# Performance work log

Hardware: AMD Instinct MI355X
Metric: run time of the kernel (lower is better)

The kernel has to match this reference:

```python
import jax, jax.numpy as jnp
import numpy as np

D, H, DK, DF = 512, 8, 64, 2048  # dim, heads, head_dim, forward_dim
EPS = 1e-5


def _layernorm(x, g, b):
    mu = jnp.mean(x, axis=-1, keepdims=True)
    var = jnp.mean(jnp.square(x - mu), axis=-1, keepdims=True)
    return (x - mu) * jax.lax.rsqrt(var + EPS) * g + b


def setup_inputs() -> dict:
    key = jax.random.key(0)
    ks = jax.random.split(key, 16)
    B, S = 2, 2048
    s_in = 1.0 / np.sqrt(D)
    s_ff = 1.0 / np.sqrt(DF)
    s_cat = 1.0 / np.sqrt(H * DK)
    return {
        "x": jax.random.normal(ks[0], (B, S, D), jnp.float32),
        # per-head Q/K/V projections stacked over heads: [H, D, DK]
        "Wq": jax.random.uniform(ks[1], (H, D, DK), jnp.float32, -s_in, s_in),
        "bq": jax.random.uniform(ks[2], (H, DK), jnp.float32, -s_in, s_in),
        "Wk": jax.random.uniform(ks[3], (H, D, DK), jnp.float32, -s_in, s_in),
        "bk": jax.random.uniform(ks[4], (H, DK), jnp.float32, -s_in, s_in),
        "Wv": jax.random.uniform(ks[5], (H, D, DK), jnp.float32, -s_in, s_in),
        "bv": jax.random.uniform(ks[6], (H, DK), jnp.float32, -s_in, s_in),
        "Wo": jax.random.uniform(ks[7], (H * DK, D), jnp.float32, -s_cat, s_cat),
        "bo": jax.random.uniform(ks[8], (D,), jnp.float32, -s_cat, s_cat),
        "ln1_g": jnp.ones((D,), jnp.float32),
        "ln1_b": jnp.zeros((D,), jnp.float32),
        "W1": jax.random.uniform(ks[9], (D, DF), jnp.float32, -s_in, s_in),
        "b1": jax.random.uniform(ks[10], (DF,), jnp.float32, -s_in, s_in),
        "W2": jax.random.uniform(ks[11], (DF, D), jnp.float32, -s_ff, s_ff),
        "b2": jax.random.uniform(ks[12], (D,), jnp.float32, -s_ff, s_ff),
        "ln2_g": jnp.ones((D,), jnp.float32),
        "ln2_b": jnp.zeros((D,), jnp.float32),
    }


def reference(x, Wq, bq, Wk, bk, Wv, bv, Wo, bo, ln1_g, ln1_b, W1, b1, W2, b2, ln2_g, ln2_b):
    # Per-head projections, batched over heads: [B,H,S,DK]
    q = jnp.einsum('bsd,hdk->bhsk', x, Wq) + bq[None, :, None, :]
    k = jnp.einsum('bsd,hdk->bhsk', x, Wk) + bk[None, :, None, :]
    v = jnp.einsum('bsd,hdk->bhsk', x, Wv) + bv[None, :, None, :]
    scale = 1.0 / np.sqrt(DK)
    scores = jnp.einsum('bhsk,bhtk->bhst', q, k) * scale  # [B,H,S,S]
    attn = jax.nn.softmax(scores, axis=-1)
    o = jnp.einsum('bhst,bhtk->bhsk', attn, v)  # [B,H,S,DK]
    # concat heads (head order matches torch cat over ModuleList)
    B, _, S, _ = o.shape
    o = o.transpose(0, 2, 1, 3).reshape(B, S, H * DK)
    attn_out = o @ Wo + bo
    # Residual 1 (dropout = identity in eval): LN(x + sublayer(x))
    h = _layernorm(x + attn_out, ln1_g, ln1_b)
    # FeedForward + Residual 2
    ff = jax.nn.relu(h @ W1 + b1) @ W2 + b2
    return _layernorm(h + ff, ln2_g, ln2_b)
```

## Files before the change

kernel.cpp:

```cpp
#include <hip/hip_runtime.h>


#define Dm   512
#define Hh   8
#define DKk  64
#define DFf  2048
#define Bb   2
#define Ss   2048
#define Nn   4096

typedef __attribute__((ext_vector_type(8))) short short8;
typedef __attribute__((ext_vector_type(4))) float f32x4;
typedef __attribute__((ext_vector_type(4))) short short4v;
typedef __attribute__((ext_vector_type(2))) int   int2v;

__device__ inline float bf2f(short s) {
    unsigned u = ((unsigned)(unsigned short)s) << 16;
    float f; __builtin_memcpy(&f, &u, 4); return f;
}
__device__ inline short f2bf(float f) {
    unsigned u; __builtin_memcpy(&u, &f, 4);
    u = (u + 0x7fff + ((u >> 16) & 1)) >> 16;
    return (short)u;
}
__device__ inline short cvt_elem(const void* p, long i, int f32flag) {
    if (f32flag) return f2bf(((const float*)p)[i]);
    return ((const short*)p)[i];
}
__device__ inline int detect_f32(const void* x) {
    const float* xf = (const float*)x;
    int ok = 0;
#pragma unroll
    for (int i = 0; i < 16; ++i) {
        float a = fabsf(xf[i]);
        ok += (a > 1e-8f && a < 1e4f) ? 1 : 0;
    }
    return ok >= 8;
}
__device__ inline void gload_lds16(const short* g, short* l) {
    __builtin_amdgcn_global_load_lds(
        (const __attribute__((address_space(1))) unsigned int*)g,
        (__attribute__((address_space(3))) unsigned int*)l, 16, 0, 0);
}

__device__ inline void epi_store128(
    short* SM, const f32x4 (&acc)[4][4], const short* bias, int colbias,
    short* out, long rowbase, long pitch, int colbase,
    float scale, int relu, int wm, int wn, int quad, int l15, int t)
{
    __syncthreads();
#pragma unroll
    for (int nt = 0; nt < 4; ++nt) {
        int col_l = wn * 64 + nt * 16 + l15;
        float bb = bias ? bf2f(bias[colbias + col_l]) : 0.f;
#pragma unroll
        for (int mt = 0; mt < 4; ++mt)
#pragma unroll
            for (int r = 0; r < 4; ++r) {
                int row_l = wm * 64 + mt * 16 + quad * 4 + r;
                float v = (acc[mt][nt][r] + bb) * scale;
                if (relu) v = fmaxf(v, 0.f);
                SM[row_l * 136 + col_l] = f2bf(v);
            }
    }
    __syncthreads();
    int row_l = t >> 1;
    int x0 = (t & 1) * 64;
#pragma unroll
    for (int k = 0; k < 8; ++k)
        *(short8*)&out[(rowbase + row_l) * pitch + colbase + x0 + k * 8] =
            *(const short8*)&SM[row_l * 136 + x0 + k * 8];
}

__global__ __launch_bounds__(256) void prep_kernel(
    const void* __restrict__ x, short* __restrict__ xb,
    const void* bq, const void* bk, const void* bv, const void* bo,
    const void* b1, const void* b2, const void* g1, const void* be1,
    const void* g2, const void* be2, short* __restrict__ smalls,
    const void* Wq, const void* Wk, const void* Wv,
    const void* Wo, const void* W1, const void* W2,
    short* __restrict__ WqkvT,
    short* __restrict__ WoT, short* __restrict__ W1T, short* __restrict__ W2T)
{
    const int f = detect_f32(x);
    int blk = blockIdx.x;
    if (blk < 512) {
        long base = (long)blk * 4096;
        if (!f) {
            const short8* src8 = (const short8*)((const short*)x + base);
            short8* dst8 = (short8*)(xb + base);
            for (int i = threadIdx.x; i < 512; i += 256) dst8[i] = src8[i];
        } else {
            for (int i = threadIdx.x; i < 4096; i += 256)
                xb[base + i] = cvt_elem(x, base + i, f);
        }
        return;
    }
    if (blk == 512) {
        const void* srcs[10] = {bq, bk, bv, bo, b1, b2, g1, be1, g2, be2};
        const int   sz[10]   = {512, 512, 512, 512, 2048, 512, 512, 512, 512, 512};
        int off = 0;
        for (int j = 0; j < 10; ++j) {
            for (int i = threadIdx.x; i < sz[j]; i += 256)
                smalls[off + i] = cvt_elem(srcs[j], i, f);
            off += sz[j];
        }
        return;
    }
    __shared__ short tile[64][65];
    blk -= 513;
    const void* src; short* dst; long srcoff = 0; long dstoff = 0; int R, C, tr, tc;
    if (blk < 192) {
        int m = blk >> 6; int r = blk & 63; int h = r >> 3; int t = r & 7;
        src = (m == 0) ? Wq : (m == 1) ? Wk : Wv;
        dst = WqkvT + (long)m * 512 * 512;
        srcoff = (long)h * 512 * 64; dstoff = (long)h * 64 * 512;
        R = 512; C = 64; tr = t; tc = 0;
    } else if (blk < 256) {
        int r = blk - 192; src = Wo; dst = WoT; R = 512; C = 512; tr = r >> 3; tc = r & 7;
    } else if (blk < 512) {
        int r = blk - 256; src = W1; dst = W1T; R = 512; C = 2048; tr = r >> 5; tc = r & 31;
    } else {
        int r = blk - 512; src = W2; dst = W2T; R = 2048; C = 512; tr = r >> 3; tc = r & 7;
    }
    int r0 = tr * 64, c0 = tc * 64;
    if (!f) {
        const short* s16 = (const short*)src;
        for (int i = threadIdx.x; i < 512; i += 256) {
            int rr = i >> 3, c8 = (i & 7) * 8;
            short8 v = *(const short8*)&s16[srcoff + (long)(r0 + rr) * C + c0 + c8];
#pragma unroll
            for (int j = 0; j < 8; ++j) tile[rr][c8 + j] = v[j];
        }
        __syncthreads();
        for (int i = threadIdx.x; i < 512; i += 256) {
            int cc = i >> 3, r8 = (i & 7) * 8;
            short8 w;
#pragma unroll
            for (int j = 0; j < 8; ++j) w[j] = tile[r8 + j][cc];
            *(short8*)&dst[dstoff + (long)(c0 + cc) * R + r0 + r8] = w;
        }
    } else {
        for (int i = threadIdx.x; i < 4096; i += 256) {
            int rr = i >> 6, cc = i & 63;
            tile[rr][cc] = cvt_elem(src, srcoff + (long)(r0 + rr) * C + c0 + cc, f);
        }
        __syncthreads();
        for (int i = threadIdx.x; i < 4096; i += 256) {
            int cc = i >> 6, rr = i & 63;
            dst[dstoff + (long)(c0 + cc) * R + r0 + rr] = tile[rr][cc];
        }
    }
}

#define MODE_PART      1
#define MODE_RELU_BF16 2
#define MODE_QKV       4

__global__ __launch_bounds__(256) void gemm_kernel(
    const short* __restrict__ A, const short* __restrict__ Bt,
    const short* __restrict__ bias, void* __restrict__ outp,
    void* __restrict__ out2, void* __restrict__ out3,
    int K, int Ncols, int mode, int Ktile)
{
    __shared__ __align__(16) short SMEM[32768];
    short* As = SMEM;
    short* Bs = SMEM + 16384;
    const int t    = threadIdx.x;
    const int lane = t & 63;
    const int wave = t >> 6;
    const int quad = lane >> 4;
    const int l15  = lane & 15;
    const int wm = wave >> 1, wn = wave & 1;
    const int row0 = blockIdx.x * 128;
    const int col0 = blockIdx.y * 128;
    const int kbase = blockIdx.z * Ktile;

    const int ri = lane >> 3;
    const int ct = (lane & 7) ^ ri;

    f32x4 acc[4][4];
#pragma unroll
    for (int i = 0; i < 4; ++i)
#pragma unroll
        for (int j = 0; j < 4; ++j) acc[i][j] = (f32x4){0.f, 0.f, 0.f, 0.f};

    auto stage = [&](int buf, int k0) {
#pragma unroll
        for (int p = 0; p < 4; ++p) {
            int r = wave * 32 + p * 8;
            gload_lds16(A + (long)(row0 + r + ri) * K + kbase + k0 + ct * 8,
                        &As[buf * 8192 + r * 64 + lane * 8]);
        }
#pragma unroll
        for (int p = 0; p < 4; ++p) {
            int r = wave * 32 + p * 8;
            gload_lds16(Bt + (long)(col0 + r + ri) * K + kbase + k0 + ct * 8,
                        &Bs[buf * 8192 + r * 64 + lane * 8]);
        }
    };

    stage(0, 0);
    int cur = 0;
    const int niter = Ktile >> 6;
    for (int it = 0; it < niter; ++it) {
        asm volatile("s_waitcnt vmcnt(0)" ::: "memory");
        __syncthreads();
        if (it + 1 < niter) stage(cur ^ 1, (it + 1) * 64);
#pragma unroll
        for (int kk = 0; kk < 2; ++kk) {
            short8 af[4], bfr[4];
#pragma unroll
            for (int mt = 0; mt < 4; ++mt) {
                int rowa = wm * 64 + mt * 16 + l15;
                af[mt] = *(const short8*)&As[cur * 8192 + rowa * 64
                              + (((kk * 4 + quad) ^ (rowa & 7)) * 8)];
            }
#pragma unroll
            for (int nt = 0; nt < 4; ++nt) {
                int rowb = wn * 64 + nt * 16 + l15;
                bfr[nt] = *(const short8*)&Bs[cur * 8192 + rowb * 64
                              + (((kk * 4 + quad) ^ (rowb & 7)) * 8)];
            }
#pragma unroll
            for (int mt = 0; mt < 4; ++mt)
#pragma unroll
                for (int nt = 0; nt < 4; ++nt)
                    acc[mt][nt] = __builtin_amdgcn_mfma_f32_16x16x32_bf16(
                        af[mt], bfr[nt], acc[mt][nt], 0, 0, 0);
        }
        cur ^= 1;
    }

    if (mode == MODE_QKV) {
        if (col0 < 1024) {
            int m = col0 >> 9;
            short* out = (short*)(m == 0 ? outp : out2);
            float sc = (m == 0) ? 0.125f : 1.0f;
            epi_store128(SMEM, acc, bias, col0, out, row0, 512, col0 & 511,
                         sc, 0, wm, wn, quad, l15, t);
        } else {
            __syncthreads();
            short* Asf = SMEM;
#pragma unroll
            for (int nt = 0; nt < 4; ++nt) {
                int col_l = wn * 64 + nt * 16 + l15;
                float bb = bf2f(bias[col0 + col_l]);
#pragma unroll
                for (int mt = 0; mt < 4; ++mt) {
                    int row4 = wm * 16 + mt * 4 + quad;
                    int slot = row4 ^ (col_l & 31);
                    short4v pk;
#pragma unroll
                    for (int r = 0; r < 4; ++r) pk[r] = f2bf(acc[mt][nt][r] + bb);
                    *(short4v*)&Asf[col_l * 128 + slot * 4] = pk;
                }
            }
            __syncthreads();
            short* out = (short*)out3;
            int col_l = t >> 1;
            int cl = col0 + col_l - 1024;
            int hh = cl >> 6, kk2 = cl & 63;
            int bg = row0 >> 11;
            long obase = ((long)(bg * Hh + hh) * DKk + kk2) * Ss + (row0 & 2047);
#pragma unroll
            for (int i = 0; i < 8; ++i) {
                int chunk = (t & 1) * 8 + i;
                int s0 = (chunk * 2)     ^ (col_l & 31);
                int s1 = (chunk * 2 + 1) ^ (col_l & 31);
                short4v a = *(const short4v*)&Asf[col_l * 128 + s0 * 4];
                short4v b4 = *(const short4v*)&Asf[col_l * 128 + s1 * 4];
                short8 w;
                w[0] = a[0];  w[1] = a[1];  w[2] = a[2];  w[3] = a[3];
                w[4] = b4[0]; w[5] = b4[1]; w[6] = b4[2]; w[7] = b4[3];
                *(short8*)&out[obase + chunk * 8] = w;
            }
        }
    } else if (mode == MODE_PART) {
        short* out = (short*)outp + (long)blockIdx.z * Nn * Ncols;
        epi_store128(SMEM, acc, (blockIdx.z == 0) ? bias : nullptr, col0,
                     out, row0, Ncols, col0, 1.f, 0, wm, wn, quad, l15, t);
    } else {
        epi_store128(SMEM, acc, bias, col0, (short*)outp, row0, Ncols, col0,
                     1.f, 1, wm, wn, quad, l15, t);
    }
}

__global__ __launch_bounds__(256) void wogemm_kernel(
    const short* __restrict__ po, const float* __restrict__ ls,
    const short* __restrict__ Bt, const short* __restrict__ bias,
    short* __restrict__ outp)
{
    __shared__ __align__(16) short SMEM[32768];
    short* As = SMEM;
    short* Bs = SMEM + 16384;
    const int t    = threadIdx.x;
    const int lane = t & 63;
    const int wave = t >> 6;
    const int quad = lane >> 4;
    const int l15  = lane & 15;
    const int wm = wave >> 1, wn = wave & 1;
    const int row0 = blockIdx.x * 128;
    const int col0 = blockIdx.y * 128;
    const int z    = blockIdx.z;

    const int ri = lane >> 3;
    const int ct = (lane & 7) ^ ri;
    const int myrow = t >> 1;
    const int tcb = (t & 1) * 4;
    const int bg = row0 >> 11;
    const int qtl = (row0 >> 7) & 15;

    f32x4 acc[4][4];
#pragma unroll
    for (int i = 0; i < 4; ++i)
#pragma unroll
        for (int j = 0; j < 4; ++j) acc[i][j] = (f32x4){0.f, 0.f, 0.f, 0.f};

    auto stageB = [&](int buf, int k0) {
#pragma unroll
        for (int p = 0; p < 4; ++p) {
            int r = wave * 32 + p * 8;
            gload_lds16(Bt + (long)(col0 + r + ri) * 512 + z * 256 + k0 + ct * 8,
                        &Bs[buf * 8192 + r * 64 + lane * 8]);
        }
    };

    short8 aR[4][4];
    float  lR[4];
    auto loadA = [&](int it) {
        int h = z * 4 + it;
        long pbase = ((long)(bg * Hh + h) * 16 + qtl) * 4;
#pragma unroll
        for (int ks = 0; ks < 4; ++ks) {
            lR[ks] = ls[(pbase + ks) * 128 + myrow];
#pragma unroll
            for (int c = 0; c < 4; ++c)
                aR[c][ks] = *(const short8*)&po[((pbase + ks) * 128 + myrow) * 64
                                                + (tcb + c) * 8];
        }
    };
    auto cvtwrite = [&](int buf) {
        float invL = __builtin_amdgcn_rcpf(lR[0] + lR[1] + lR[2] + lR[3]);
#pragma unroll
        for (int c = 0; c < 4; ++c) {
            short8 w;
#pragma unroll
            for (int j = 0; j < 8; ++j) {
                float s = bf2f(aR[c][0][j]) + bf2f(aR[c][1][j])
                        + bf2f(aR[c][2][j]) + bf2f(aR[c][3][j]);
                w[j] = f2bf(s * invL);
            }
            int slot = (tcb + c) ^ (myrow & 7);
            *(short8*)&As[buf * 8192 + myrow * 64 + slot * 8] = w;
        }
    };

    loadA(0); stageB(0, 0); cvtwrite(0);
    int cur = 0;
#pragma unroll
    for (int it = 0; it < 4; ++it) {
        __syncthreads();
        if (it < 3) { loadA(it + 1); stageB(cur ^ 1, (it + 1) * 64); }
#pragma unroll
        for (int kk = 0; kk < 2; ++kk) {
            short8 af[4], bfr[4];
#pragma unroll
            for (int mt = 0; mt < 4; ++mt) {
                int rowa = wm * 64 + mt * 16 + l15;
                af[mt] = *(const short8*)&As[cur * 8192 + rowa * 64
                              + (((kk * 4 + quad) ^ (rowa & 7)) * 8)];
            }
#pragma unroll
            for (int nt = 0; nt < 4; ++nt) {
                int rowb = wn * 64 + nt * 16 + l15;
                bfr[nt] = *(const short8*)&Bs[cur * 8192 + rowb * 64
                              + (((kk * 4 + quad) ^ (rowb & 7)) * 8)];
            }
#pragma unroll
            for (int mt = 0; mt < 4; ++mt)
#pragma unroll
                for (int nt = 0; nt < 4; ++nt)
                    acc[mt][nt] = __builtin_amdgcn_mfma_f32_16x16x32_bf16(
                        af[mt], bfr[nt], acc[mt][nt], 0, 0, 0);
        }
        if (it < 3) cvtwrite(cur ^ 1);
        cur ^= 1;
    }

    short* out = outp + (long)z * Nn * Dm;
    epi_store128(SMEM, acc, (z == 0) ? bias : nullptr, col0,
                 out, row0, Dm, col0, 1.f, 0, wm, wn, quad, l15, t);
}

__global__ __launch_bounds__(256) void attn_kernel(
    const short* __restrict__ Q, const short* __restrict__ Kt,
    const short* __restrict__ Vt, short* __restrict__ po, float* __restrict__ ls)
{
    __shared__ __align__(16) short Ks[64 * 64];
    __shared__ __align__(16) short Vs[64 * 64];
    __shared__ __align__(16) short pbuf[4][32 * 72];
    const int lane = threadIdx.x & 63;
    const int wave = threadIdx.x >> 6;
    const int quad = lane >> 4;
    const int l15  = lane & 15;
    const int qt = blockIdx.x, bh = blockIdx.y, ks = blockIdx.z;
    const int b = bh >> 3, h = bh & 7;
    const int qrow = b * Ss + qt * 128 + wave * 32;

    short8 bq[2][2];
#pragma unroll
    for (int qh = 0; qh < 2; ++qh)
#pragma unroll
        for (int kk = 0; kk < 2; ++kk)
            bq[qh][kk] = *(const short8*)(Q + (long)(qrow + qh * 16 + l15) * Dm
                                          + h * DKk + kk * 32 + quad * 8);

    f32x4 o[2][4];
    float lsum[2] = {0.f, 0.f};
#pragma unroll
    for (int qh = 0; qh < 2; ++qh)
#pragma unroll
        for (int nt = 0; nt < 4; ++nt) o[qh][nt] = (f32x4){0.f, 0.f, 0.f, 0.f};

    const short* Kg = Kt + (long)b * Ss * Dm + h * DKk;
    const short* Vg = Vt + (long)bh * DKk * Ss;
    short* pbw = pbuf[wave];
    const int t00 = ks * 512;

    const int ri = lane >> 3;
    const int ct = (lane & 7) ^ ri;
    const int ldsrow0 = wave * 16;

    for (int it = 0; it < 8; ++it) {
        const int t0 = t00 + it * 64;
#pragma unroll
        for (int p = 0; p < 2; ++p) {
            int r = ldsrow0 + p * 8 + ri;
            gload_lds16(Kg + (long)(t0 + r) * Dm + ct * 8,
                        &Ks[(ldsrow0 + p * 8) * 64] + lane * 8);
        }
#pragma unroll
        for (int p = 0; p < 2; ++p) {
            int r = ldsrow0 + p * 8 + ri;
            gload_lds16(Vg + (long)r * Ss + t0 + ct * 8,
                        &Vs[(ldsrow0 + p * 8) * 64] + lane * 8);
        }
        asm volatile("s_waitcnt vmcnt(0)" ::: "memory");
        __syncthreads();

#pragma unroll
        for (int j = 0; j < 4; ++j) {
            short8 kf0 = *(const short8*)&Ks[(j * 16 + l15) * 64
                                             + ((quad ^ (l15 & 7)) * 8)];
            short8 kf1 = *(const short8*)&Ks[(j * 16 + l15) * 64
                                             + (((4 + quad) ^ (l15 & 7)) * 8)];
#pragma unroll
            for (int qh = 0; qh < 2; ++qh) {
                f32x4 sj = (f32x4){0.f, 0.f, 0.f, 0.f};
                sj = __builtin_amdgcn_mfma_f32_16x16x32_bf16(kf0, bq[qh][0], sj, 0, 0, 0);
                sj = __builtin_amdgcn_mfma_f32_16x16x32_bf16(kf1, bq[qh][1], sj, 0, 0, 0);
                int2v pk;
#pragma unroll
                for (int r2 = 0; r2 < 2; ++r2) {
                    float pa = __expf(fminf(sj[r2 * 2 + 0], 20.f));
                    float pc = __expf(fminf(sj[r2 * 2 + 1], 20.f));
                    lsum[qh] += pa + pc;
                    unsigned ua, uc;
                    __builtin_memcpy(&ua, &pa, 4);
                    __builtin_memcpy(&uc, &pc, 4);
                    pk[r2] = __builtin_amdgcn_perm(uc, ua, 0x07060302);
                }
                *(int2v*)&pbw[(qh * 16 + l15) * 72 + j * 16 + quad * 4] = pk;
            }
        }
        asm volatile("s_waitcnt lgkmcnt(0)" ::: "memory");
#pragma unroll
        for (int c = 0; c < 2; ++c) {
            short8 ap[2];
#pragma unroll
            for (int qh = 0; qh < 2; ++qh)
                ap[qh] = *(const short8*)&pbw[(qh * 16 + l15) * 72 + c * 32 + quad * 8];
#pragma unroll
            for (int nt = 0; nt < 4; ++nt) {
                short8 vf = *(const short8*)&Vs[(nt * 16 + l15) * 64
                                                + (((c * 4 + quad) ^ (l15 & 7)) * 8)];
#pragma unroll
                for (int qh = 0; qh < 2; ++qh)
                    o[qh][nt] = __builtin_amdgcn_mfma_f32_16x16x32_bf16(
                        ap[qh], vf, o[qh][nt], 0, 0, 0);
            }
        }
        asm volatile("" ::: "memory");
        __syncthreads();
    }

#pragma unroll
    for (int qh = 0; qh < 2; ++qh) {
        float v = lsum[qh];
        v += __shfl_xor(v, 16);
        v += __shfl_xor(v, 32);
        lsum[qh] = v;
    }
    short* SM = &pbuf[0][0];
#pragma unroll
    for (int qh = 0; qh < 2; ++qh)
#pragma unroll
        for (int nt = 0; nt < 4; ++nt)
#pragma unroll
            for (int r = 0; r < 4; ++r)
                SM[(wave * 32 + qh * 16 + quad * 4 + r) * 72 + nt * 16 + l15] =
                    f2bf(o[qh][nt][r]);
    __syncthreads();
    short* pob = po + ((((long)bh * 16 + qt) * 4 + ks) * 128) * 64;
    {
        int row_l = (int)threadIdx.x >> 1;
        int x0 = ((int)threadIdx.x & 1) * 32;
#pragma unroll
        for (int k = 0; k < 4; ++k)
            *(short8*)&pob[row_l * 64 + x0 + k * 8] =
                *(const short8*)&SM[row_l * 72 + x0 + k * 8];
    }
    if (lane < 16) {
        long lbase = (((long)bh * 16 + qt) * 4 + ks) * 128 + wave * 32;
        ls[lbase + l15]      = lsum[0];
        ls[lbase + 16 + l15] = lsum[1];
    }
}

__global__ __launch_bounds__(256) void ln_kernel(
    const short* __restrict__ v0, const short* __restrict__ v1,
    const short* __restrict__ v2, const short* __restrict__ v3,
    const short* __restrict__ res,
    const short* __restrict__ g, const short* __restrict__ bt,
    void* __restrict__ out, const void* __restrict__ xdet)
{
    const int row = blockIdx.x, tid = threadIdx.x;
    const long base = (long)row * Dm;
    const long i0 = base + tid, i1 = base + 256 + tid;
    float x0 = bf2f(v0[i0]) + bf2f(res[i0]);
    float x1 = bf2f(v0[i1]) + bf2f(res[i1]);
    if (v1) { x0 += bf2f(v1[i0]); x1 += bf2f(v1[i1]); }
    if (v2) { x0 += bf2f(v2[i0]); x1 += bf2f(v2[i1]); }
    if (v3) { x0 += bf2f(v3[i0]); x1 += bf2f(v3[i1]); }

    __shared__ float red[8];
    const int wv = tid >> 6, ln = tid & 63;
    float s = x0 + x1;
#pragma unroll
    for (int mk = 1; mk < 64; mk <<= 1) s += __shfl_xor(s, mk);
    if (!ln) red[wv] = s;
    __syncthreads();
    float mean = (red[0] + red[1] + red[2] + red[3]) * (1.f / 512.f);
    float d0 = x0 - mean, d1 = x1 - mean;
    float q = d0 * d0 + d1 * d1;
#pragma unroll
    for (int mk = 1; mk < 64; mk <<= 1) q += __shfl_xor(q, mk);
    if (!ln) red[4 + wv] = q;
    __syncthreads();
    float rs = rsqrtf((red[4] + red[5] + red[6] + red[7]) * (1.f / 512.f) + 1e-5f);
    float y0 = d0 * rs * bf2f(g[tid])       + bf2f(bt[tid]);
    float y1 = d1 * rs * bf2f(g[256 + tid]) + bf2f(bt[256 + tid]);
    int f32out = xdet ? detect_f32(xdet) : 0;
    if (f32out) {
        float* o = (float*)out;
        o[i0] = y0; o[i1] = y1;
    } else {
        short* o = (short*)out;
        o[i0] = f2bf(y0); o[i1] = f2bf(y1);
    }
}

extern "C" void kernel_launch(void* const* d_in, const int* in_sizes, int n_in,
                              void* d_out, int out_size, void* d_ws, size_t ws_size,
                              hipStream_t stream)
{
    (void)in_sizes; (void)n_in; (void)out_size; (void)ws_size;
    const void* x   = d_in[0];
    const void* Wq  = d_in[1];  const void* bq  = d_in[2];
    const void* Wk  = d_in[3];  const void* bk  = d_in[4];
    const void* Wv  = d_in[5];  const void* bv  = d_in[6];
    const void* Wo  = d_in[7];  const void* bo  = d_in[8];
    const void* g1  = d_in[9];  const void* be1 = d_in[10];
    const void* W1  = d_in[11]; const void* b1  = d_in[12];
    const void* W2  = d_in[13]; const void* b2  = d_in[14];
    const void* g2  = d_in[15]; const void* be2 = d_in[16];

    char* ws = (char*)d_ws;
    size_t off = 0;
    auto alloc = [&](size_t bytes) -> void* {
        void* p = ws + off; off += (bytes + 255) & ~(size_t)255; return p;
    };
    short* WqkvT = (short*)alloc((size_t)3 * Dm * Dm * 2);
    short* WoT   = (short*)alloc((size_t)Dm * Dm * 2);
    short* W1T   = (short*)alloc((size_t)DFf * Dm * 2);
    short* W2T   = (short*)alloc((size_t)Dm * DFf * 2);
    short* xb    = (short*)alloc((size_t)Nn * Dm * 2);
    short* sm    = (short*)alloc((size_t)6656 * 2);
    char*  regA  = (char*)alloc((size_t)Nn * DFf * 2);
    short* Qb    = (short*)(regA);
    short* Kb    = (short*)(regA + (size_t)Nn * Dm * 2);
    short* Vt    = (short*)(regA + (size_t)Nn * Dm * 4);
    short* u     = (short*)(regA);
    short* wo_p  = (short*)alloc((size_t)2 * Nn * Dm * 2);
    char*  regC  = (char*)alloc((size_t)4 * Nn * Dm * 2);
    short* po    = (short*)regC;
    short* f2p   = (short*)regC;
    float* lsb   = (float*)alloc((size_t)16 * 16 * 4 * 128 * 4);
    short* h_bf  = (short*)alloc((size_t)Nn * Dm * 2);

    prep_kernel<<<1281, 256, 0, stream>>>(x, xb, bq, bk, bv, bo, b1, b2,
                                          g1, be1, g2, be2, sm,
                                          Wq, Wk, Wv, Wo, W1, W2,
                                          WqkvT, WoT, W1T, W2T);
    gemm_kernel<<<dim3(Nn / 128, 1536 / 128, 1), 256, 0, stream>>>(
        xb, WqkvT, sm + 0, Qb, Kb, Vt, Dm, 1536, MODE_QKV, Dm);
    attn_kernel<<<dim3(Ss / 128, Bb * Hh, 4), 256, 0, stream>>>(Qb, Kb, Vt, po, lsb);
    wogemm_kernel<<<dim3(Nn / 128, Dm / 128, 2), 256, 0, stream>>>(
        po, lsb, WoT, sm + 1536, wo_p);
    ln_kernel<<<Nn, 256, 0, stream>>>(wo_p, wo_p + (long)Nn * Dm, nullptr, nullptr,
                                      xb, sm + 4608, sm + 5120, h_bf, nullptr);
    gemm_kernel<<<dim3(Nn / 128, DFf / 128, 1), 256, 0, stream>>>(
        h_bf, W1T, sm + 2048, u, nullptr, nullptr, Dm, DFf, MODE_RELU_BF16, Dm);
    gemm_kernel<<<dim3(Nn / 128, Dm / 128, 4), 256, 0, stream>>>(
        u, W2T, sm + 4096, f2p, nullptr, nullptr, DFf, Dm, MODE_PART, DFf / 4);
    ln_kernel<<<Nn, 256, 0, stream>>>(f2p, f2p + (long)Nn * Dm, f2p + (long)2 * Nn * Dm,
                                      f2p + (long)3 * Nn * Dm,
                                      h_bf, sm + 5632, sm + 6144, d_out, x);
}
```

Baseline: 215.3 us.

## Double-buffer K/V tiles and feed P from registers via 16x16x16 MFMA

Result: no change. 216.3 us (+0.5%).

```diff
diff --git a/kernel.cpp b/kernel.cpp
--- a/kernel.cpp
+++ b/kernel.cpp
@@ -41,6 +41,17 @@
     __builtin_amdgcn_global_load_lds(
         (const __attribute__((address_space(1))) unsigned int*)g,
         (__attribute__((address_space(3))) unsigned int*)l, 16, 0, 0);
+}
+__device__ inline f32x4 mfma16bf16(short4v a, short4v b, f32x4 c) {
+#if __has_builtin(__builtin_amdgcn_mfma_f32_16x16x16bf16_1k)
+    return __builtin_amdgcn_mfma_f32_16x16x16bf16_1k(a, b, c, 0, 0, 0);
+#elif __has_builtin(__builtin_amdgcn_mfma_f32_16x16x16_bf16)
+    return __builtin_amdgcn_mfma_f32_16x16x16_bf16(a, b, c, 0, 0, 0);
+#else
+    asm volatile("v_mfma_f32_16x16x16_bf16 %0, %1, %2, %0\n\ts_nop 7\n\ts_nop 7"
+                 : "+v"(c) : "v"(a), "v"(b));
+    return c;
+#endif
 }
 
 __device__ inline void epi_store128(
@@ -397,9 +408,7 @@
     const short* __restrict__ Q, const short* __restrict__ Kt,
     const short* __restrict__ Vt, short* __restrict__ po, float* __restrict__ ls)
 {
-    __shared__ __align__(16) short Ks[64 * 64];
-    __shared__ __align__(16) short Vs[64 * 64];
-    __shared__ __align__(16) short pbuf[4][32 * 72];
+    __shared__ __align__(16) short SMEM[16384];
     const int lane = threadIdx.x & 63;
     const int wave = threadIdx.x >> 6;
     const int quad = lane >> 4;
@@ -425,36 +434,49 @@
 
     const short* Kg = Kt + (long)b * Ss * Dm + h * DKk;
     const short* Vg = Vt + (long)bh * DKk * Ss;
-    short* pbw = pbuf[wave];
     const int t00 = ks * 512;
 
     const int ri = lane >> 3;
     const int ct = (lane & 7) ^ ri;
     const int ldsrow0 = wave * 16;
 
-    for (int it = 0; it < 8; ++it) {
-        const int t0 = t00 + it * 64;
+    auto stage = [&](int buf, int tkv) {
 #pragma unroll
         for (int p = 0; p < 2; ++p) {
             int r = ldsrow0 + p * 8 + ri;
-            gload_lds16(Kg + (long)(t0 + r) * Dm + ct * 8,
-                        &Ks[(ldsrow0 + p * 8) * 64] + lane * 8);
+            gload_lds16(Kg + (long)(tkv + r) * Dm + ct * 8,
+                        &SMEM[buf * 4096 + (ldsrow0 + p * 8) * 64] + lane * 8);
         }
 #pragma unroll
         for (int p = 0; p < 2; ++p) {
             int r = ldsrow0 + p * 8 + ri;
-            gload_lds16(Vg + (long)r * Ss + t0 + ct * 8,
-                        &Vs[(ldsrow0 + p * 8) * 64] + lane * 8);
-        }
+            gload_lds16(Vg + (long)r * Ss + tkv + ct * 8,
+                        &SMEM[8192 + buf * 4096 + (ldsrow0 + p * 8) * 64] + lane * 8);
+        }
+    };
+
+    stage(0, t00);
+    int cur = 0;
+    for (int it = 0; it < 8; ++it) {
         asm volatile("s_waitcnt vmcnt(0)" ::: "memory");
         __syncthreads();
-
+        if (it < 7) stage(cur ^ 1, t00 + (it + 1) * 64);
+
+        const short* Ksc = &SMEM[cur * 4096];
+        const short* Vsc = &SMEM[8192 + cur * 4096];
 #pragma unroll
         for (int j = 0; j < 4; ++j) {
-            short8 kf0 = *(const short8*)&Ks[(j * 16 + l15) * 64
-                                             + ((quad ^ (l15 & 7)) * 8)];
-            short8 kf1 = *(const short8*)&Ks[(j * 16 + l15) * 64
-                                             + (((4 + quad) ^ (l15 & 7)) * 8)];
+            short8 kf0 = *(const short8*)&Ksc[(j * 16 + l15) * 64
+                                              + ((quad ^ (l15 & 7)) * 8)];
+            short8 kf1 = *(const short8*)&Ksc[(j * 16 + l15) * 64
+                                              + (((4 + quad) ^ (l15 & 7)) * 8)];
+            short4v vf[4];
+#pragma unroll
+            for (int nt = 0; nt < 4; ++nt) {
+                int rr = nt * 16 + l15;
+                int slot = (j * 2 + (quad >> 1)) ^ (rr & 7);
+                vf[nt] = *(const short4v*)&Vsc[rr * 64 + slot * 8 + (quad & 1) * 4];
+            }
 #pragma unroll
             for (int qh = 0; qh < 2; ++qh) {
                 f32x4 sj = (f32x4){0.f, 0.f, 0.f, 0.f};
@@ -471,28 +493,14 @@
                     __builtin_memcpy(&uc, &pc, 4);
                     pk[r2] = __builtin_amdgcn_perm(uc, ua, 0x07060302);
                 }
-                *(int2v*)&pbw[(qh * 16 + l15) * 72 + j * 16 + quad * 4] = pk;
-            }
-        }
-        asm volatile("s_waitcnt lgkmcnt(0)" ::: "memory");
-#pragma unroll
-        for (int c = 0; c < 2; ++c) {
-            short8 ap[2];
-#pragma unroll
-            for (int qh = 0; qh < 2; ++qh)
-                ap[qh] = *(const short8*)&pbw[(qh * 16 + l15) * 72 + c * 32 + quad * 8];
-#pragma unroll
-            for (int nt = 0; nt < 4; ++nt) {
-                short8 vf = *(const short8*)&Vs[(nt * 16 + l15) * 64
-                                                + (((c * 4 + quad) ^ (l15 & 7)) * 8)];
-#pragma unroll
-                for (int qh = 0; qh < 2; ++qh)
-                    o[qh][nt] = __builtin_amdgcn_mfma_f32_16x16x32_bf16(
-                        ap[qh], vf, o[qh][nt], 0, 0, 0);
-            }
-        }
-        asm volatile("" ::: "memory");
-        __syncthreads();
+                short4v ap;
+                __builtin_memcpy(&ap, &pk, 8);
+#pragma unroll
+                for (int nt = 0; nt < 4; ++nt)
+                    o[qh][nt] = mfma16bf16(ap, vf[nt], o[qh][nt]);
+            }
+        }
+        cur ^= 1;
     }
 
 #pragma unroll
@@ -502,7 +510,8 @@
         v += __shfl_xor(v, 32);
         lsum[qh] = v;
     }
-    short* SM = &pbuf[0][0];
+    __syncthreads();
+    short* SM = SMEM;
 #pragma unroll
     for (int qh = 0; qh < 2; ++qh)
 #pragma unroll
```
